# Optimization experiments

Hardware: AMD Instinct MI355X
Metric: run time of the kernel (lower is better)

## Reference

```python
import math
import jax, jax.numpy as jnp
import numpy as np

ALPHA = 1000.0
N_LAMBDA = 1.0


def setup_inputs() -> dict:
    key = jax.random.key(0)
    k1, k2 = jax.random.split(key)
    xyz1 = jax.random.normal(k1, (4, 8192, 3), dtype=jnp.float32)  # prediction
    xyz2 = jax.random.normal(k2, (4, 8192, 3), dtype=jnp.float32)  # ground truth
    return {"xyz1": xyz1, "xyz2": xyz2}


def _nn(a, b):
    """For each point in a [B,Na,3], squared dist + index of nearest point in b [B,Nb,3]."""
    a2 = jnp.sum(a * a, axis=-1)[:, :, None]          # [B,Na,1]
    b2 = jnp.sum(b * b, axis=-1)[:, None, :]          # [B,1,Nb]
    d = a2 + b2 - 2.0 * jnp.einsum('bnd,bmd->bnm', a, b)  # [B,Na,Nb]
    return jnp.min(d, axis=-1), jnp.argmin(d, axis=-1)


def reference(xyz1, xyz2):
    B, n_x, _ = xyz1.shape
    n_gt = xyz2.shape[1]
    frac_21 = n_gt / n_x

    # torch code calls ChamferFunction.apply(xyz2, xyz1):
    # dist1/idx1 are for gt points (idx1 indexes into xyz1, range n_x),
    # dist2/idx2 are for pred points (idx2 indexes into xyz2, range n_gt).
    dist1, idx1 = _nn(xyz2, xyz1)   # [B, n_gt]
    dist2, idx2 = _nn(xyz1, xyz2)   # [B, n_x]

    exp_dist1 = jnp.exp(-dist1 * ALPHA)
    exp_dist2 = jnp.exp(-dist2 * ALPHA)

    batch = jnp.arange(B)[:, None]

    # how many gt points picked each pred point
    count1 = jnp.zeros((B, n_x), jnp.int32).at[batch, idx1].add(1)
    weight1 = jnp.take_along_axis(count1, idx1, axis=1).astype(jnp.float32) ** N_LAMBDA
    weight1 = 1.0 / jnp.maximum(frac_21 / weight1 + 1e-6, 1.0)
    loss1 = jnp.mean(1.0 - exp_dist1 * weight1, axis=1)

    # how many pred points picked each gt point
    count2 = jnp.zeros((B, n_gt), jnp.int32).at[batch, idx2].add(1)
    weight2 = jnp.take_along_axis(count2, idx2, axis=1).astype(jnp.float32) ** N_LAMBDA
    weight2 = 1.0 / (math.ceil(frac_21) * weight2 + 1e-6)
    loss2 = jnp.mean(1.0 - exp_dist2 * weight2, axis=1)

    return jnp.mean((loss1 + loss2) / 2.0)
```

## Files before the change

kernel.cpp:

```cpp
#include <hip/hip_runtime.h>
#include <cstdint>
#include <cstddef>

#define BATCH 4
#define NPTS 8192
#define BLOCK 256
#define NKEYS (2 * BATCH * NPTS)
#define CHUNK_M 1024
#define NTILES (CHUNK_M / 32)
#define QPB 128


typedef __attribute__((ext_vector_type(8))) short bf16x8;
typedef __attribute__((ext_vector_type(16))) float f32x16;

__device__ __forceinline__ float halfnorm(float px, float py, float pz) {
    return 0.5f * fmaf(pz, pz, fmaf(py, py, px * px));
}
__device__ __forceinline__ unsigned int mono_f32(float f) {
    unsigned int u = __float_as_uint(f);
    return u ^ (unsigned int)(((int)u >> 31) | 0x80000000);
}
__device__ __forceinline__ unsigned int bf16_rne(float f) {
    unsigned int u = __float_as_uint(f);
    u = u + 0x7FFFu + ((u >> 16) & 1u);
    return u >> 16;
}

__global__ void __launch_bounds__(BLOCK) prep_kernel(
        const float* __restrict__ xyz1,
        const float* __restrict__ xyz2,
        uint4* __restrict__ planes,
        unsigned int* __restrict__ counts,
        float* __restrict__ esum,
        float* __restrict__ out) {
    const int gtid = blockIdx.x * BLOCK + threadIdx.x;
    const int arr = gtid >> 15;
    const int rem = gtid & 32767;
    const int b = rem >> 13;
    const int i = rem & (NPTS - 1);
    const float* src = ((arr == 0) ? xyz1 : xyz2) + (size_t)(b * NPTS + i) * 3;
    const float px = src[0], py = src[1], pz = src[2];
    const float ph = halfnorm(px, py, pz);

    const unsigned xh = bf16_rne(px);
    const unsigned xl = bf16_rne(px - __uint_as_float(xh << 16));
    const unsigned yh = bf16_rne(py);
    const unsigned yl = bf16_rne(py - __uint_as_float(yh << 16));
    const unsigned zh = bf16_rne(pz);
    const unsigned zl = bf16_rne(pz - __uint_as_float(zh << 16));
    const unsigned hh = bf16_rne(ph);
    const unsigned hl = bf16_rne(ph - __uint_as_float(hh << 16));

    uint4 w;
    w.x = xh | (yh << 16);
    w.y = zh | (xl << 16);
    w.z = yl | (zl << 16);
    w.w = hh | (hl << 16);
    planes[(size_t)(arr * 4 + b) * NPTS + i] = w;

    counts[gtid] = 0u;
    esum[gtid]   = 0.0f;
    if (gtid == 0) out[0] = 1.0f;
}

__global__ void __launch_bounds__(BLOCK, 4) nn_kernel(
        const uint4* __restrict__ planes,
        unsigned long long* __restrict__ keys) {
    __shared__ uint4 Alds[CHUNK_M];
    const int tid = threadIdx.x;
    const int wav = tid >> 6;
    const int lane = tid & 63;
    const int col = lane & 31;
    const int h = lane >> 5;
    const int qt = blockIdx.x;
    const int ct = blockIdx.y;
    const int zb = blockIdx.z;
    const int b = zb & 3;
    const int dir = zb >> 2;
    const int g_db = (dir == 0) ? b : 4 + b;
    const int g_q  = (dir == 0) ? 4 + b : b;

    const uint4* asrc = planes + (size_t)g_db * NPTS + ct * CHUNK_M;
#pragma unroll
    for (int it = 0; it < CHUNK_M / BLOCK; ++it)
        Alds[it * BLOCK + tid] = asrc[it * BLOCK + tid];

    const int qidx = qt * QPB + wav * 32 + col;
    const uint4 qw = planes[(size_t)g_q * NPTS + qidx];
    unsigned b0, b1, b2, b3;
    if (h == 0) {
        const unsigned n0 = qw.x ^ 0x80008000u;
        b0 = n0;
        b1 = ((qw.y ^ 0x8000u) & 0xFFFFu) | (n0 << 16);
        b2 = (n0 >> 16) | ((qw.y ^ 0x8000u) << 16);
        b3 = 0x3F803F80u;
    } else {
        b0 = ((qw.y >> 16) | (qw.z << 16)) ^ 0x80008000u;
        b1 = (qw.z >> 16) ^ 0x8000u;
        b2 = 0u;
        b3 = 0u;
    }
    uint4 bw; bw.x = b0; bw.y = b1; bw.z = b2; bw.w = b3;
    const bf16x8 bf = __builtin_bit_cast(bf16x8, bw);
    const f32x16 zacc = {};

    __syncthreads();

    float bd = 3.4e38f;
    int bt = 0;
#pragma unroll 2
    for (int t = 0; t < NTILES; ++t) {
        const uint4 aw = Alds[t * 32 + col];
        const bf16x8 af = __builtin_bit_cast(bf16x8, aw);
        const f32x16 s =
            __builtin_amdgcn_mfma_f32_32x32x16_bf16(af, bf, zacc, 0, 0, 0);
        float m0 = fminf(fminf(s[0], s[1]), s[2]);
        float m1 = fminf(fminf(s[3], s[4]), s[5]);
        float m2 = fminf(fminf(s[6], s[7]), s[8]);
        float m3 = fminf(fminf(s[9], s[10]), s[11]);
        float m4 = fminf(fminf(s[12], s[13]), s[14]);
        float m5 = fminf(fminf(s[15], m0), m1);
        float m6 = fminf(fminf(m2, m3), m4);
        const float m = fminf(m5, m6);
        if (m < bd) { bd = m; bt = t; }
    }

    unsigned long long key =
        ((unsigned long long)mono_f32(bd) << 32) |
        (unsigned)(ct * CHUNK_M + (bt << 5) + (h << 2));
    const unsigned long long other = __shfl_down(key, 32);
    if (h == 0) {
        if (other < key) key = other;
        atomicMin(&keys[(size_t)zb * NPTS + qidx], key);
    }
}

__global__ void __launch_bounds__(BLOCK) mid_kernel(
        const float* __restrict__ xyz1,
        const float* __restrict__ xyz2,
        const unsigned long long* __restrict__ keys,
        unsigned int* __restrict__ counts,
        float* __restrict__ esum) {
    const int gtid = blockIdx.x * BLOCK + threadIdx.x;
    const int group = gtid >> 13;
    const int q   = gtid & (NPTS - 1);
    const int b   = group & 3;
    const int dir = group >> 2;
    const float* q_ptr = (dir == 0) ? xyz2 : xyz1;
    const float* d_ptr = (dir == 0) ? xyz1 : xyz2;

    const unsigned long long key = keys[gtid];
    const int base = ((int)(unsigned int)key) & ((NPTS - 32) | 4);

    const float* qp = q_ptr + (size_t)(b * NPTS + q) * 3;
    const float qx = qp[0], qy = qp[1], qz = qp[2];

    float bestd = 3.4e38f;
    int bestr = 0;
#pragma unroll
    for (int j = 0; j < 4; ++j) {
        const int r0 = base + 8 * j;
        const float4* g4 = (const float4*)(d_ptr + (size_t)(b * NPTS + r0) * 3);
        const float4 t0 = g4[0], t1 = g4[1], t2 = g4[2];
        const float px[4] = {t0.x, t0.w, t1.z, t2.y};
        const float py[4] = {t0.y, t1.x, t1.w, t2.z};
        const float pz[4] = {t0.z, t1.y, t2.x, t2.w};
#pragma unroll
        for (int k = 0; k < 4; ++k) {
            const float dx = qx - px[k], dy = qy - py[k], dz = qz - pz[k];
            const float d = dx * dx + dy * dy + dz * dz;
            if (d < bestd) { bestd = d; bestr = r0 + k; }
        }
    }

    const float e = expf(-1000.0f * bestd);
    atomicAdd(&counts[(size_t)group * NPTS + bestr], 1u);
    atomicAdd(&esum[(size_t)group * NPTS + bestr], e);
}

__global__ void __launch_bounds__(BLOCK) final_kernel(
        const unsigned int* __restrict__ counts,
        const float* __restrict__ esum,
        float* __restrict__ out) {
    __shared__ float red[4];
    const int gtid = blockIdx.x * BLOCK + threadIdx.x;
    const int dir = gtid >> 15;

    const float c = (float)counts[gtid];
    const float e = esum[gtid];
    float w;
    if (dir == 0) w = 1.0f / fmaxf(1.0f / c + 1e-6f, 1.0f);
    else          w = 1.0f / (c + 1e-6f);
    float term = -w * e;

#pragma unroll
    for (int off = 32; off > 0; off >>= 1)
        term += __shfl_down(term, off);
    const int lane = threadIdx.x & 63;
    const int wid  = threadIdx.x >> 6;
    if (lane == 0) red[wid] = term;
    __syncthreads();
    if (threadIdx.x == 0) {
        float t = red[0] + red[1] + red[2] + red[3];
        atomicAdd(out, t * (1.0f / 65536.0f));
    }
}

extern "C" void kernel_launch(void* const* d_in, const int* in_sizes, int n_in,
                              void* d_out, int out_size, void* d_ws, size_t ws_size,
                              hipStream_t stream) {
    const float* xyz1 = (const float*)d_in[0];
    const float* xyz2 = (const float*)d_in[1];
    float* out = (float*)d_out;

    unsigned long long* keys = (unsigned long long*)d_ws;
    unsigned int* counts = (unsigned int*)((char*)d_ws + (size_t)NKEYS * 8);
    float* esum = (float*)((char*)d_ws + (size_t)NKEYS * 12);
    uint4* planes = (uint4*)((char*)d_ws + (size_t)NKEYS * 16);

    prep_kernel<<<NKEYS / BLOCK, BLOCK, 0, stream>>>(xyz1, xyz2, planes,
                                                     counts, esum, out);
    nn_kernel<<<dim3(NPTS / QPB, NPTS / CHUNK_M, 2 * BATCH), BLOCK, 0, stream>>>(
        planes, keys);
    mid_kernel<<<NKEYS / BLOCK, BLOCK, 0, stream>>>(xyz1, xyz2, keys, counts, esum);
    final_kernel<<<NKEYS / BLOCK, BLOCK, 0, stream>>>(counts, esum, out);
}
```

Before: 89.95 us.

## Fuse point preprocessing into NN kernel and halve refinement candidates

```diff
diff --git a/kernel.cpp b/kernel.cpp
--- a/kernel.cpp
+++ b/kernel.cpp
@@ -27,46 +27,13 @@
     return u >> 16;
 }
 
-__global__ void __launch_bounds__(BLOCK) prep_kernel(
+__global__ void __launch_bounds__(BLOCK, 4) nn_kernel(
         const float* __restrict__ xyz1,
         const float* __restrict__ xyz2,
-        uint4* __restrict__ planes,
+        unsigned long long* __restrict__ keys,
         unsigned int* __restrict__ counts,
         float* __restrict__ esum,
         float* __restrict__ out) {
-    const int gtid = blockIdx.x * BLOCK + threadIdx.x;
-    const int arr = gtid >> 15;
-    const int rem = gtid & 32767;
-    const int b = rem >> 13;
-    const int i = rem & (NPTS - 1);
-    const float* src = ((arr == 0) ? xyz1 : xyz2) + (size_t)(b * NPTS + i) * 3;
-    const float px = src[0], py = src[1], pz = src[2];
-    const float ph = halfnorm(px, py, pz);
-
-    const unsigned xh = bf16_rne(px);
-    const unsigned xl = bf16_rne(px - __uint_as_float(xh << 16));
-    const unsigned yh = bf16_rne(py);
-    const unsigned yl = bf16_rne(py - __uint_as_float(yh << 16));
-    const unsigned zh = bf16_rne(pz);
-    const unsigned zl = bf16_rne(pz - __uint_as_float(zh << 16));
-    const unsigned hh = bf16_rne(ph);
-    const unsigned hl = bf16_rne(ph - __uint_as_float(hh << 16));
-
-    uint4 w;
-    w.x = xh | (yh << 16);
-    w.y = zh | (xl << 16);
-    w.z = yl | (zl << 16);
-    w.w = hh | (hl << 16);
-    planes[(size_t)(arr * 4 + b) * NPTS + i] = w;
-
-    counts[gtid] = 0u;
-    esum[gtid]   = 0.0f;
-    if (gtid == 0) out[0] = 1.0f;
-}
-
-__global__ void __launch_bounds__(BLOCK, 4) nn_kernel(
-        const uint4* __restrict__ planes,
-        unsigned long long* __restrict__ keys) {
     __shared__ uint4 Alds[CHUNK_M];
     const int tid = threadIdx.x;
     const int wav = tid >> 6;
@@ -78,26 +45,59 @@
     const int zb = blockIdx.z;
     const int b = zb & 3;
     const int dir = zb >> 2;
-    const int g_db = (dir == 0) ? b : 4 + b;
-    const int g_q  = (dir == 0) ? 4 + b : b;
-
-    const uint4* asrc = planes + (size_t)g_db * NPTS + ct * CHUNK_M;
-#pragma unroll
-    for (int it = 0; it < CHUNK_M / BLOCK; ++it)
-        Alds[it * BLOCK + tid] = asrc[it * BLOCK + tid];
+    const float* d_raw = (dir == 0) ? xyz1 : xyz2;
+    const float* q_raw = (dir == 0) ? xyz2 : xyz1;
+
+    const int bid = (zb * 8 + ct) * 64 + qt;
+    if (tid < 16) {
+        counts[(size_t)bid * 16 + tid] = 0u;
+        esum[(size_t)bid * 16 + tid]   = 0.0f;
+    }
+    if (bid == 0 && tid == 0) out[0] = 1.0f;
+
+    const int chunk0 = ct * CHUNK_M;
+#pragma unroll
+    for (int it = 0; it < CHUNK_M / BLOCK; ++it) {
+        const int i = it * BLOCK + tid;
+        const float* p = d_raw + (size_t)(b * NPTS + chunk0 + i) * 3;
+        const float px = p[0], py = p[1], pz = p[2];
+        const float ph = halfnorm(px, py, pz);
+        const unsigned xh = bf16_rne(px);
+        const unsigned xl = bf16_rne(px - __uint_as_float(xh << 16));
+        const unsigned yh = bf16_rne(py);
+        const unsigned yl = bf16_rne(py - __uint_as_float(yh << 16));
+        const unsigned zh = bf16_rne(pz);
+        const unsigned zl = bf16_rne(pz - __uint_as_float(zh << 16));
+        const unsigned hh = bf16_rne(ph);
+        const unsigned hl = bf16_rne(ph - __uint_as_float(hh << 16));
+        uint4 w;
+        w.x = xh | (yh << 16);
+        w.y = zh | (xl << 16);
+        w.z = yl | (zl << 16);
+        w.w = hh | (hl << 16);
+        Alds[i] = w;
+    }
 
     const int qidx = qt * QPB + wav * 32 + col;
-    const uint4 qw = planes[(size_t)g_q * NPTS + qidx];
+    const float* qp = q_raw + (size_t)(b * NPTS + qidx) * 3;
+    const float qx = qp[0], qy = qp[1], qz = qp[2];
+    const unsigned qxh = bf16_rne(qx);
+    const unsigned qxl = bf16_rne(qx - __uint_as_float(qxh << 16));
+    const unsigned qyh = bf16_rne(qy);
+    const unsigned qyl = bf16_rne(qy - __uint_as_float(qyh << 16));
+    const unsigned qzh = bf16_rne(qz);
+    const unsigned qzl = bf16_rne(qz - __uint_as_float(qzh << 16));
     unsigned b0, b1, b2, b3;
     if (h == 0) {
-        const unsigned n0 = qw.x ^ 0x80008000u;
-        b0 = n0;
-        b1 = ((qw.y ^ 0x8000u) & 0xFFFFu) | (n0 << 16);
-        b2 = (n0 >> 16) | ((qw.y ^ 0x8000u) << 16);
+        const unsigned nx = qxh ^ 0x8000u, ny = qyh ^ 0x8000u, nz = qzh ^ 0x8000u;
+        b0 = nx | (ny << 16);
+        b1 = nz | (nx << 16);
+        b2 = ny | (nz << 16);
         b3 = 0x3F803F80u;
     } else {
-        b0 = ((qw.y >> 16) | (qw.z << 16)) ^ 0x80008000u;
-        b1 = (qw.z >> 16) ^ 0x8000u;
+        const unsigned nx = qxl ^ 0x8000u, ny = qyl ^ 0x8000u, nz = qzl ^ 0x8000u;
+        b0 = nx | (ny << 16);
+        b1 = nz;
         b2 = 0u;
         b3 = 0u;
     }
@@ -107,28 +107,34 @@
 
     __syncthreads();
 
-    float bd = 3.4e38f;
-    int bt = 0;
+    float bdL = 3.4e38f, bdU = 3.4e38f;
+    int   btL = 0,       btU = 0;
 #pragma unroll 2
     for (int t = 0; t < NTILES; ++t) {
         const uint4 aw = Alds[t * 32 + col];
         const bf16x8 af = __builtin_bit_cast(bf16x8, aw);
         const f32x16 s =
             __builtin_amdgcn_mfma_f32_32x32x16_bf16(af, bf, zacc, 0, 0, 0);
-        float m0 = fminf(fminf(s[0], s[1]), s[2]);
-        float m1 = fminf(fminf(s[3], s[4]), s[5]);
-        float m2 = fminf(fminf(s[6], s[7]), s[8]);
-        float m3 = fminf(fminf(s[9], s[10]), s[11]);
-        float m4 = fminf(fminf(s[12], s[13]), s[14]);
-        float m5 = fminf(fminf(s[15], m0), m1);
-        float m6 = fminf(fminf(m2, m3), m4);
-        const float m = fminf(m5, m6);
-        if (m < bd) { bd = m; bt = t; }
-    }
+        const float l0 = fminf(fminf(s[0], s[1]), s[2]);
+        const float l1 = fminf(fminf(s[3], s[4]), s[5]);
+        const float l2 = fminf(s[6], s[7]);
+        const float mL = fminf(fminf(l0, l1), l2);
+        const float u0 = fminf(fminf(s[8], s[9]), s[10]);
+        const float u1 = fminf(fminf(s[11], s[12]), s[13]);
+        const float u2 = fminf(s[14], s[15]);
+        const float mU = fminf(fminf(u0, u1), u2);
+        if (mL < bdL) { bdL = mL; btL = t; }
+        if (mU < bdU) { bdU = mU; btU = t; }
+    }
+
+    float bd; int code;
+    if (bdU < bdL) { bd = bdU; code = (btU << 5) + 16; }
+    else           { bd = bdL; code = (btL << 5); }
+    code += h << 2;
 
     unsigned long long key =
         ((unsigned long long)mono_f32(bd) << 32) |
-        (unsigned)(ct * CHUNK_M + (bt << 5) + (h << 2));
+        (unsigned)(chunk0 + code);
     const unsigned long long other = __shfl_down(key, 32);
     if (h == 0) {
         if (other < key) key = other;
@@ -151,7 +157,7 @@
     const float* d_ptr = (dir == 0) ? xyz1 : xyz2;
 
     const unsigned long long key = keys[gtid];
-    const int base = ((int)(unsigned int)key) & ((NPTS - 32) | 4);
+    const int base = ((int)(unsigned int)key) & ((NPTS - 32) | 20);
 
     const float* qp = q_ptr + (size_t)(b * NPTS + q) * 3;
     const float qx = qp[0], qy = qp[1], qz = qp[2];
@@ -159,7 +165,7 @@
     float bestd = 3.4e38f;
     int bestr = 0;
 #pragma unroll
-    for (int j = 0; j < 4; ++j) {
+    for (int j = 0; j < 2; ++j) {
         const int r0 = base + 8 * j;
         const float4* g4 = (const float4*)(d_ptr + (size_t)(b * NPTS + r0) * 3);
         const float4 t0 = g4[0], t1 = g4[1], t2 = g4[2];
@@ -217,12 +223,9 @@
     unsigned long long* keys = (unsigned long long*)d_ws;
     unsigned int* counts = (unsigned int*)((char*)d_ws + (size_t)NKEYS * 8);
     float* esum = (float*)((char*)d_ws + (size_t)NKEYS * 12);
-    uint4* planes = (uint4*)((char*)d_ws + (size_t)NKEYS * 16);
-
-    prep_kernel<<<NKEYS / BLOCK, BLOCK, 0, stream>>>(xyz1, xyz2, planes,
-                                                     counts, esum, out);
+
     nn_kernel<<<dim3(NPTS / QPB, NPTS / CHUNK_M, 2 * BATCH), BLOCK, 0, stream>>>(
-        planes, keys);
+        xyz1, xyz2, keys, counts, esum, out);
     mid_kernel<<<NKEYS / BLOCK, BLOCK, 0, stream>>>(xyz1, xyz2, keys, counts, esum);
     final_kernel<<<NKEYS / BLOCK, BLOCK, 0, stream>>>(counts, esum, out);
 }
```

New measurement: 92.18 us. 1.02x slower.
